# Kernel tuning notes

Measured on AMD Instinct MI355X. Metric: run time of the kernel, lower is better.

## Reference

```python
import jax, jax.numpy as jnp
import numpy as np

EPS = 1e-5
NUM_HEADS = 3


def _ln(x, g, b):
    m = jnp.mean(x, axis=-1, keepdims=True)
    v = jnp.mean((x - m) ** 2, axis=-1, keepdims=True)
    return (x - m) * jax.lax.rsqrt(v + EPS) * g + b


def setup_inputs() -> dict:
    key = jax.random.key(0)
    ks = jax.random.split(key, 8)
    Bn, N, C = 256, 197, 192           # graph nodes, tokens per node, embed_dim
    E = 1024                           # edges
    hid = int(C * 4.0)                 # mlp hidden
    def w(k, shape, fan_in):
        return (jax.random.normal(k, shape, jnp.float32) / np.sqrt(fan_in)).astype(jnp.float32)
    return {
        "x": jax.random.normal(ks[0], (Bn, N, C), jnp.float32),
        "egde": jax.random.randint(ks[1], (2, E), 0, Bn),
        "norm1_g": jnp.ones((C,), jnp.float32),
        "norm1_b": jnp.zeros((C,), jnp.float32),
        "qkv_w": w(ks[2], (3 * C, C), C),          # Linear(dim, 3*dim, bias=False)
        "proj_w": w(ks[3], (C, C), C),
        "proj_b": jnp.zeros((C,), jnp.float32),
        "norm2_g": jnp.ones((C,), jnp.float32),
        "norm2_b": jnp.zeros((C,), jnp.float32),
        "fc1_w": w(ks[4], (hid, C), C),
        "fc1_b": jnp.zeros((hid,), jnp.float32),
        "fc2_w": w(ks[5], (C, hid), hid),
        "fc2_b": jnp.zeros((C,), jnp.float32),
    }


def reference(x, egde, norm1_g, norm1_b, qkv_w, proj_w, proj_b,
              norm2_g, norm2_b, fc1_w, fc1_b, fc2_w, fc2_b):
    Bn, N, C = x.shape
    H = NUM_HEADS
    hd = C // H
    scale = hd ** -0.5

    # --- MEConv2 ---
    xn = _ln(x, norm1_g, norm1_b)
    qkv = (xn @ qkv_w.T).reshape(Bn, N, 3, H, hd)
    src, dst = egde[0], egde[1]        # x_j = source, aggregation index = target
    xi = qkv[dst]                      # [E, N, 3, H, hd]
    xj = qkv[src]
    q = xi[:, :, 0]                    # [E, N, H, hd] (from destination)
    v = xi[:, :, 2]                    # note: v comes from x_i, as in the source
    k = xj[:, :, 1]                    # key from source node
    attn = jnp.einsum('enhd,emhd->ehnm', q, k) * scale   # [E, H, N, N]
    attn = jax.nn.softmax(attn, axis=-1)
    msg = jnp.einsum('ehnm,emhd->enhd', attn, v).reshape(-1, N, C)
    msg = msg @ proj_w.T + proj_b      # [E, N, C]
    # scatter-mean over destination nodes (empty nodes -> 0, like torch scatter)
    agg = jax.ops.segment_sum(msg, dst, num_segments=Bn)
    cnt = jax.ops.segment_sum(jnp.ones(dst.shape, x.dtype), dst, num_segments=Bn)
    y = agg / jnp.maximum(cnt, 1.0)[:, None, None]

    # --- residual + MLP ---
    x = x + y
    h = _ln(x, norm2_g, norm2_b)
    h = jax.nn.gelu(h @ fc1_w.T + fc1_b, approximate=False)  # torch nn.GELU = exact
    h = h @ fc2_w.T + fc2_b
    return x + h
```

## Files before the change

### kernel.cpp

```cpp
#include <hip/hip_runtime.h>
#include <hip/hip_bf16.h>
#include <cstddef>


typedef __attribute__((ext_vector_type(8))) short bf8_t;
typedef __attribute__((ext_vector_type(4))) float f4_t;

__device__ __forceinline__ float bf2f(unsigned short u) {
  union { unsigned int i; float f; } x; x.i = ((unsigned int)u) << 16; return x.f;
}
__device__ __forceinline__ unsigned short f2bf(float f) {
  unsigned int u = __builtin_bit_cast(unsigned int, f);
  u = (u + 0x7FFFu + ((u >> 16) & 1u)) >> 16;
  return (unsigned short)u;
}
__device__ __forceinline__ unsigned int cvt_pk_bf16(float a, float b) {
  unsigned int r;
  asm("v_cvt_pk_bf16_f32 %0, %1, %2" : "=v"(r) : "v"(a), "v"(b));
  return r;
}

__global__ __launch_bounds__(256) void f2bf_kernel(const float* __restrict__ src,
                                                   unsigned short* __restrict__ dst, int n) {
  int i = blockIdx.x * 256 + threadIdx.x;
  if (i < n) dst[i] = f2bf(src[i]);
}

__global__ __launch_bounds__(256) void ln_bf16_kernel(const float* __restrict__ X,
    const float* __restrict__ g, const float* __restrict__ b,
    unsigned short* __restrict__ Y) {
  int row = blockIdx.x * 4 + (threadIdx.x >> 6);
  int lane = threadIdx.x & 63;
  const float* xr = X + (size_t)row * 192;
  float v0 = xr[lane], v1 = xr[lane + 64], v2 = xr[lane + 128];
  float s = v0 + v1 + v2, ss = v0 * v0 + v1 * v1 + v2 * v2;
#pragma unroll
  for (int o = 32; o > 0; o >>= 1) { s += __shfl_xor(s, o, 64); ss += __shfl_xor(ss, o, 64); }
  float mean = s * (1.f / 192.f);
  float var = ss * (1.f / 192.f) - mean * mean;
  float r = rsqrtf(var + 1e-5f);
  unsigned short* yr = Y + (size_t)row * 192;
  yr[lane]       = f2bf((v0 - mean) * r * g[lane]       + b[lane]);
  yr[lane + 64]  = f2bf((v1 - mean) * r * g[lane + 64]  + b[lane + 64]);
  yr[lane + 128] = f2bf((v2 - mean) * r * g[lane + 128] + b[lane + 128]);
}

template<int MODE, int NK>
__global__ __launch_bounds__(256) void gemm_bf16(
    const unsigned short* __restrict__ A, const unsigned short* __restrict__ W,
    const float* __restrict__ bias, const float* __restrict__ xres,
    const int* __restrict__ cntg, void* __restrict__ Cout,
    unsigned short* __restrict__ Cvt, int ldc) {
  constexpr int LDA = 200;
  __shared__ unsigned short As[128 * LDA];
  __shared__ unsigned short Ws[64 * LDA];
  const int tid = threadIdx.x;
  const int m0 = blockIdx.x * 128, n0 = blockIdx.y * 64;
  const int wave = tid >> 6, lane = tid & 63;
  const int mfrag = lane & 15, quad = lane >> 4;
  const int K = NK * 192;

  f4_t acc[2][4];
#pragma unroll
  for (int i = 0; i < 2; ++i)
#pragma unroll
    for (int j = 0; j < 4; ++j) acc[i][j] = (f4_t){0.f, 0.f, 0.f, 0.f};

  for (int kc = 0; kc < NK; ++kc) {
    __syncthreads();
#pragma unroll
    for (int it = 0; it < 12; ++it) {
      int idx = it * 256 + tid;
      int r = idx / 24, c = idx % 24;
      *(float4*)(As + r * LDA + c * 8) =
          *(const float4*)(A + (size_t)(m0 + r) * K + kc * 192 + c * 8);
    }
#pragma unroll
    for (int it = 0; it < 6; ++it) {
      int idx = it * 256 + tid;
      int r = idx / 24, c = idx % 24;
      *(float4*)(Ws + r * LDA + c * 8) =
          *(const float4*)(W + (size_t)(n0 + r) * K + kc * 192 + c * 8);
    }
    __syncthreads();
#pragma unroll
    for (int ks = 0; ks < 6; ++ks) {
      bf8_t a0 = *(const bf8_t*)(As + (wave * 32 + mfrag) * LDA + ks * 32 + quad * 8);
      bf8_t a1 = *(const bf8_t*)(As + (wave * 32 + 16 + mfrag) * LDA + ks * 32 + quad * 8);
#pragma unroll
      for (int nt = 0; nt < 4; ++nt) {
        bf8_t bf = *(const bf8_t*)(Ws + (nt * 16 + mfrag) * LDA + ks * 32 + quad * 8);
        acc[0][nt] = __builtin_amdgcn_mfma_f32_16x16x32_bf16(a0, bf, acc[0][nt], 0, 0, 0);
        acc[1][nt] = __builtin_amdgcn_mfma_f32_16x16x32_bf16(a1, bf, acc[1][nt], 0, 0, 0);
      }
    }
  }

#pragma unroll
  for (int mt = 0; mt < 2; ++mt)
#pragma unroll
    for (int nt = 0; nt < 4; ++nt)
#pragma unroll
      for (int reg = 0; reg < 4; ++reg) {
        int row = m0 + wave * 32 + mt * 16 + quad * 4 + reg;
        int col = n0 + nt * 16 + mfrag;
        float v = acc[mt][nt][reg];
        if constexpr (MODE == 0) {
          if (col < 384) {
            ((unsigned short*)Cout)[(size_t)row * 384 + col] = f2bf(v);
          } else {
            int cc = col - 384, hh = cc >> 6, dd = cc & 63;
            int bb = row / 197, tt = row - bb * 197;
            Cvt[((size_t)(bb * 3 + hh) * 64 + dd) * 200 + tt] = f2bf(v);
          }
        } else if constexpr (MODE == 1) {
          int c = cntg[row / 197];
          v = (c > 0) ? v / (float)c + bias[col] : 0.f;
          v += xres[(size_t)row * 192 + col];
          ((float*)Cout)[(size_t)row * ldc + col] = v;
        } else if constexpr (MODE == 2) {
          v += bias[col];
          v = 0.5f * v * (1.f + erff(v * 0.70710678118654752f));
          ((unsigned short*)Cout)[(size_t)row * ldc + col] = f2bf(v);
        } else {
          v += bias[col] + xres[(size_t)row * 192 + col];
          ((float*)Cout)[(size_t)row * ldc + col] = v;
        }
      }
}

__global__ __launch_bounds__(512) void attnA_kernel(
    const unsigned short* __restrict__ qk, const unsigned short* __restrict__ vtg,
    const int* __restrict__ edge, unsigned short* __restrict__ msgbuf) {
  const int e = blockIdx.x, h = blockIdx.y;
  const int s = edge[e], b = edge[1024 + e];
  __shared__ unsigned short Ks[208 * 72];
  __shared__ unsigned short Vt[64 * 232];
  __shared__ unsigned short Ps[8][640];
  const int tid = threadIdx.x;
  const int wave = tid >> 6, lane = tid & 63;
  const int mfrag = lane & 15, quad = lane >> 4;

  for (int i = tid; i < 197 * 8; i += 512) {
    int m = i >> 3, c8 = i & 7;
    *(float4*)(Ks + m * 72 + c8 * 8) =
        *(const float4*)(qk + (size_t)(s * 197 + m) * 384 + 192 + h * 64 + c8 * 8);
  }
  for (int i = tid; i < 64 * 25; i += 512) {
    int d = i / 25, c8 = i - d * 25;
    *(float4*)(Vt + d * 232 + c8 * 8) =
        *(const float4*)(vtg + ((size_t)(b * 3 + h) * 64 + d) * 200 + c8 * 8);
  }
  __syncthreads();
  for (int i = tid; i < 64 * 35; i += 512) {
    int d = i / 35, kk = 197 + (i - d * 35);
    Vt[d * 232 + kk] = 0;
  }
  __syncthreads();

  for (int st = wave; st < 13; st += 8) {
    const int m0 = st * 16;
    const size_t qrow = (size_t)(b * 197 + min(m0 + mfrag, 196)) * 384 + h * 64;
    bf8_t a0 = *(const bf8_t*)(qk + qrow + quad * 8);
    bf8_t a1 = *(const bf8_t*)(qk + qrow + 32 + quad * 8);

    f4_t S[13];
#pragma unroll
    for (int nt = 0; nt < 13; ++nt) {
      bf8_t k0 = *(const bf8_t*)(Ks + (nt * 16 + mfrag) * 72 + quad * 8);
      bf8_t k1 = *(const bf8_t*)(Ks + (nt * 16 + mfrag) * 72 + 32 + quad * 8);
      f4_t z = (f4_t){0.f, 0.f, 0.f, 0.f};
      z = __builtin_amdgcn_mfma_f32_16x16x32_bf16(a0, k0, z, 0, 0, 0);
      S[nt] = __builtin_amdgcn_mfma_f32_16x16x32_bf16(a1, k1, z, 0, 0, 0);
    }

#pragma unroll
    for (int reg = 0; reg < 4; ++reg)
      S[12][reg] = (mfrag < 5) ? S[12][reg] : -1e30f;

    float mx[4] = {-1e30f, -1e30f, -1e30f, -1e30f};
#pragma unroll
    for (int nt = 0; nt < 13; ++nt)
#pragma unroll
      for (int reg = 0; reg < 4; ++reg) mx[reg] = fmaxf(mx[reg], S[nt][reg]);
#pragma unroll
    for (int off = 1; off < 16; off <<= 1)
#pragma unroll
      for (int reg = 0; reg < 4; ++reg) mx[reg] = fmaxf(mx[reg], __shfl_xor(mx[reg], off, 64));

    constexpr float CEXP = 0.18033688011112042f;
    float sum[4] = {0.f, 0.f, 0.f, 0.f};
#pragma unroll
    for (int nt = 0; nt < 13; ++nt)
#pragma unroll
      for (int reg = 0; reg < 4; ++reg) {
        float p = exp2f((S[nt][reg] - mx[reg]) * CEXP);
        S[nt][reg] = p;
        sum[reg] += p;
      }
#pragma unroll
    for (int off = 1; off < 16; off <<= 1)
#pragma unroll
      for (int reg = 0; reg < 4; ++reg) sum[reg] += __shfl_xor(sum[reg], off, 64);
    float inv[4];
#pragma unroll
    for (int reg = 0; reg < 4; ++reg) inv[reg] = __builtin_amdgcn_rcpf(sum[reg]);

    f4_t o[4];
#pragma unroll
    for (int dt = 0; dt < 4; ++dt) o[dt] = (f4_t){0.f, 0.f, 0.f, 0.f};
    unsigned short* buf = Ps[wave];
#pragma unroll
    for (int kt = 0; kt < 7; ++kt) {
#pragma unroll
      for (int reg = 0; reg < 4; ++reg) {
        float p0 = S[kt * 2][reg];
        float p1 = (kt * 2 + 1 < 13) ? S[kt * 2 + 1][reg] : 0.f;
        unsigned int u = cvt_pk_bf16(p0, p1);
        buf[(quad * 4 + reg) * 40 + mfrag]      = (unsigned short)u;
        buf[(quad * 4 + reg) * 40 + 16 + mfrag] = (unsigned short)(u >> 16);
      }
      bf8_t pf = *(const bf8_t*)(buf + mfrag * 40 + quad * 8);
#pragma unroll
      for (int dt = 0; dt < 4; ++dt) {
        bf8_t vf = *(const bf8_t*)(Vt + (dt * 16 + mfrag) * 232 + kt * 32 + quad * 8);
        o[dt] = __builtin_amdgcn_mfma_f32_16x16x32_bf16(pf, vf, o[dt], 0, 0, 0);
      }
    }

#pragma unroll
    for (int dt = 0; dt < 4; dt += 2)
#pragma unroll
      for (int reg = 0; reg < 4; ++reg) {
        int q = m0 + quad * 4 + reg;
        unsigned int u = cvt_pk_bf16(o[dt][reg] * inv[reg], o[dt + 1][reg] * inv[reg]);
        if (q < 197) {
          size_t base = (size_t)e * 37824 + q * 192 + h * 64 + dt * 16 + mfrag;
          msgbuf[base]      = (unsigned short)u;
          msgbuf[base + 16] = (unsigned short)(u >> 16);
        }
      }
  }
}

__global__ __launch_bounds__(256) void aggregate_kernel(
    const unsigned short* __restrict__ msgbuf, const int* __restrict__ edge,
    unsigned short* __restrict__ agg, int* __restrict__ cntg) {
  const int b = blockIdx.x, chunk = blockIdx.y;
  __shared__ int list[1024];
  __shared__ int lc;
  const int tid = threadIdx.x;
  if (tid == 0) lc = 0;
  __syncthreads();
  for (int e = tid; e < 1024; e += 256)
    if (edge[1024 + e] == b) { int p = atomicAdd(&lc, 1); list[p] = e; }
  __syncthreads();
  const int cnt = lc;
  if (chunk == 0 && tid == 0) cntg[b] = cnt;
  const int base = chunk * 9456;
  for (int i8 = tid; i8 < 1182; i8 += 256) {
    int i = base + i8 * 8;
    float sum[8];
#pragma unroll
    for (int kk = 0; kk < 8; ++kk) sum[kk] = 0.f;
    for (int j = 0; j < cnt; ++j) {
      float4 t = *(const float4*)(msgbuf + (size_t)list[j] * 37824 + i);
      const unsigned short* u = (const unsigned short*)&t;
#pragma unroll
      for (int kk = 0; kk < 8; ++kk) sum[kk] += bf2f(u[kk]);
    }
    unsigned short o[8];
#pragma unroll
    for (int kk = 0; kk < 8; ++kk) o[kk] = f2bf(sum[kk]);
    *(float4*)(agg + (size_t)b * 37824 + i) = *(const float4*)o;
  }
}

extern "C" void kernel_launch(void* const* d_in, const int* in_sizes, int n_in,
                              void* d_out, int out_size, void* d_ws, size_t ws_size,
                              hipStream_t stream) {
  const float* x      = (const float*)d_in[0];
  const int*   edge   = (const int*)d_in[1];
  const float* n1g    = (const float*)d_in[2];
  const float* n1b    = (const float*)d_in[3];
  const float* qkv_w  = (const float*)d_in[4];
  const float* proj_w = (const float*)d_in[5];
  const float* proj_b = (const float*)d_in[6];
  const float* n2g    = (const float*)d_in[7];
  const float* n2b    = (const float*)d_in[8];
  const float* fc1_w  = (const float*)d_in[9];
  const float* fc1_b  = (const float*)d_in[10];
  const float* fc2_w  = (const float*)d_in[11];
  const float* fc2_b  = (const float*)d_in[12];
  float* out = (float*)d_out;

  char* ws = (char*)d_ws;
  unsigned short* msgbuf = (unsigned short*)ws;
  unsigned short* h1     = (unsigned short*)ws;
  unsigned short* qk     = (unsigned short*)(ws + 77463552);
  unsigned short* xn     = (unsigned short*)(ws + 116195328);
  unsigned short* agg    = (unsigned short*)(ws + 135561216);
  unsigned short* vtg    = (unsigned short*)(ws + 154927104);
  unsigned short* wqkv   = (unsigned short*)(ws + 174587904);
  unsigned short* wproj  = (unsigned short*)(ws + 174809088);
  unsigned short* wfc1   = (unsigned short*)(ws + 174882816);
  unsigned short* wfc2   = (unsigned short*)(ws + 175177728);
  int*            cntg   = (int*)           (ws + 175472640);

  dim3 blk(256);
  f2bf_kernel<<<dim3(432), blk, 0, stream>>>(qkv_w, wqkv, 110592);
  f2bf_kernel<<<dim3(144), blk, 0, stream>>>(proj_w, wproj, 36864);
  f2bf_kernel<<<dim3(576), blk, 0, stream>>>(fc1_w, wfc1, 147456);
  f2bf_kernel<<<dim3(576), blk, 0, stream>>>(fc2_w, wfc2, 147456);

  ln_bf16_kernel<<<dim3(12608), blk, 0, stream>>>(x, n1g, n1b, xn);
  gemm_bf16<0, 1><<<dim3(394, 9), blk, 0, stream>>>(xn, wqkv, nullptr, nullptr, nullptr, qk, vtg, 384);
  attnA_kernel<<<dim3(1024, 3), dim3(512), 0, stream>>>(qk, vtg, edge, msgbuf);
  aggregate_kernel<<<dim3(256, 4), blk, 0, stream>>>(msgbuf, edge, agg, cntg);
  gemm_bf16<1, 1><<<dim3(394, 3), blk, 0, stream>>>(agg, wproj, proj_b, x, cntg, out, nullptr, 192);
  ln_bf16_kernel<<<dim3(12608), blk, 0, stream>>>(out, n2g, n2b, xn);
  gemm_bf16<2, 1><<<dim3(394, 12), blk, 0, stream>>>(xn, wfc1, fc1_b, nullptr, nullptr, h1, nullptr, 768);
  gemm_bf16<3, 4><<<dim3(394, 3), blk, 0, stream>>>(h1, wfc2, fc2_b, out, nullptr, out, nullptr, 192);
}
```

Measured before the change: 477.3 us.

## Fuse scatter-mean into attention via float atomics, drop message buffer

The attention kernel now atomically adds normalized outputs straight into a float32 per-node aggregation buffer. This replaces the per-edge bf16 message buffer and the separate aggregate kernel, and a small kernel computes the in-degree counts. The proj GEMM reads the fp32 aggregate and converts it to bf16 while loading. Softmax row reductions switch from shuffles to DPP row rotations, and GEMM grids are swapped so N tiles vary fastest for better A reuse. The cost is a memset of the aggregate buffer, atomic contention on high-degree nodes, and nondeterministic summation order.

Result: slower. 544.5 us (+14.1%).

```diff
diff --git a/kernel.cpp b/kernel.cpp
--- a/kernel.cpp
+++ b/kernel.cpp
@@ -19,11 +19,27 @@
   asm("v_cvt_pk_bf16_f32 %0, %1, %2" : "=v"(r) : "v"(a), "v"(b));
   return r;
 }
+template<int CTRL>
+__device__ __forceinline__ float dpp_ror(float x) {
+  return __builtin_bit_cast(float,
+      __builtin_amdgcn_mov_dpp(__builtin_bit_cast(int, x), CTRL, 0xF, 0xF, false));
+}
 
 __global__ __launch_bounds__(256) void f2bf_kernel(const float* __restrict__ src,
                                                    unsigned short* __restrict__ dst, int n) {
   int i = blockIdx.x * 256 + threadIdx.x;
   if (i < n) dst[i] = f2bf(src[i]);
+}
+
+__global__ __launch_bounds__(256) void cnt_kernel(const int* __restrict__ edge,
+                                                  int* __restrict__ cntg) {
+  __shared__ int c[256];
+  int t = threadIdx.x;
+  c[t] = 0;
+  __syncthreads();
+  for (int e = t; e < 1024; e += 256) atomicAdd(&c[edge[1024 + e]], 1);
+  __syncthreads();
+  cntg[t] = c[t];
 }
 
 __global__ __launch_bounds__(256) void ln_bf16_kernel(const float* __restrict__ X,
@@ -45,9 +61,10 @@
   yr[lane + 128] = f2bf((v2 - mean) * r * g[lane + 128] + b[lane + 128]);
 }
 
-template<int MODE, int NK>
+template<int MODE, int NK, bool AF32 = false>
 __global__ __launch_bounds__(256) void gemm_bf16(
-    const unsigned short* __restrict__ A, const unsigned short* __restrict__ W,
+    const unsigned short* __restrict__ A, const float* __restrict__ Af,
+    const unsigned short* __restrict__ W,
     const float* __restrict__ bias, const float* __restrict__ xres,
     const int* __restrict__ cntg, void* __restrict__ Cout,
     unsigned short* __restrict__ Cvt, int ldc) {
@@ -55,7 +72,7 @@
   __shared__ unsigned short As[128 * LDA];
   __shared__ unsigned short Ws[64 * LDA];
   const int tid = threadIdx.x;
-  const int m0 = blockIdx.x * 128, n0 = blockIdx.y * 64;
+  const int m0 = blockIdx.y * 128, n0 = blockIdx.x * 64;
   const int wave = tid >> 6, lane = tid & 63;
   const int mfrag = lane & 15, quad = lane >> 4;
   const int K = NK * 192;
@@ -68,12 +85,25 @@
 
   for (int kc = 0; kc < NK; ++kc) {
     __syncthreads();
-#pragma unroll
-    for (int it = 0; it < 12; ++it) {
-      int idx = it * 256 + tid;
-      int r = idx / 24, c = idx % 24;
-      *(float4*)(As + r * LDA + c * 8) =
-          *(const float4*)(A + (size_t)(m0 + r) * K + kc * 192 + c * 8);
+    if constexpr (AF32) {
+#pragma unroll
+      for (int it = 0; it < 24; ++it) {
+        int idx = it * 256 + tid;
+        int r = idx / 48, c = idx % 48;
+        float4 t = *(const float4*)(Af + (size_t)(m0 + r) * K + kc * 192 + c * 4);
+        unsigned int u0 = cvt_pk_bf16(t.x, t.y);
+        unsigned int u1 = cvt_pk_bf16(t.z, t.w);
+        uint2 p; p.x = u0; p.y = u1;
+        *(uint2*)(As + r * LDA + c * 4) = p;
+      }
+    } else {
+#pragma unroll
+      for (int it = 0; it < 12; ++it) {
+        int idx = it * 256 + tid;
+        int r = idx / 24, c = idx % 24;
+        *(float4*)(As + r * LDA + c * 8) =
+            *(const float4*)(A + (size_t)(m0 + r) * K + kc * 192 + c * 8);
+      }
     }
 #pragma unroll
     for (int it = 0; it < 6; ++it) {
@@ -131,7 +161,7 @@
 
 __global__ __launch_bounds__(512) void attnA_kernel(
     const unsigned short* __restrict__ qk, const unsigned short* __restrict__ vtg,
-    const int* __restrict__ edge, unsigned short* __restrict__ msgbuf) {
+    const int* __restrict__ edge, float* __restrict__ aggF) {
   const int e = blockIdx.x, h = blockIdx.y;
   const int s = edge[e], b = edge[1024 + e];
   __shared__ unsigned short Ks[208 * 72];
@@ -184,9 +214,12 @@
 #pragma unroll
       for (int reg = 0; reg < 4; ++reg) mx[reg] = fmaxf(mx[reg], S[nt][reg]);
 #pragma unroll
-    for (int off = 1; off < 16; off <<= 1)
-#pragma unroll
-      for (int reg = 0; reg < 4; ++reg) mx[reg] = fmaxf(mx[reg], __shfl_xor(mx[reg], off, 64));
+    for (int reg = 0; reg < 4; ++reg) {
+      mx[reg] = fmaxf(mx[reg], dpp_ror<0x121>(mx[reg]));
+      mx[reg] = fmaxf(mx[reg], dpp_ror<0x122>(mx[reg]));
+      mx[reg] = fmaxf(mx[reg], dpp_ror<0x124>(mx[reg]));
+      mx[reg] = fmaxf(mx[reg], dpp_ror<0x128>(mx[reg]));
+    }
 
     constexpr float CEXP = 0.18033688011112042f;
     float sum[4] = {0.f, 0.f, 0.f, 0.f};
@@ -199,9 +232,12 @@
         sum[reg] += p;
       }
 #pragma unroll
-    for (int off = 1; off < 16; off <<= 1)
-#pragma unroll
-      for (int reg = 0; reg < 4; ++reg) sum[reg] += __shfl_xor(sum[reg], off, 64);
+    for (int reg = 0; reg < 4; ++reg) {
+      sum[reg] += dpp_ror<0x121>(sum[reg]);
+      sum[reg] += dpp_ror<0x122>(sum[reg]);
+      sum[reg] += dpp_ror<0x124>(sum[reg]);
+      sum[reg] += dpp_ror<0x128>(sum[reg]);
+    }
     float inv[4];
 #pragma unroll
     for (int reg = 0; reg < 4; ++reg) inv[reg] = __builtin_amdgcn_rcpf(sum[reg]);
@@ -229,50 +265,14 @@
     }
 
 #pragma unroll
-    for (int dt = 0; dt < 4; dt += 2)
+    for (int dt = 0; dt < 4; ++dt)
 #pragma unroll
       for (int reg = 0; reg < 4; ++reg) {
         int q = m0 + quad * 4 + reg;
-        unsigned int u = cvt_pk_bf16(o[dt][reg] * inv[reg], o[dt + 1][reg] * inv[reg]);
-        if (q < 197) {
-          size_t base = (size_t)e * 37824 + q * 192 + h * 64 + dt * 16 + mfrag;
-          msgbuf[base]      = (unsigned short)u;
-          msgbuf[base + 16] = (unsigned short)(u >> 16);
-        }
-      }
-  }
-}
-
-__global__ __launch_bounds__(256) void aggregate_kernel(
-    const unsigned short* __restrict__ msgbuf, const int* __restrict__ edge,
-    unsigned short* __restrict__ agg, int* __restrict__ cntg) {
-  const int b = blockIdx.x, chunk = blockIdx.y;
-  __shared__ int list[1024];
-  __shared__ int lc;
-  const int tid = threadIdx.x;
-  if (tid == 0) lc = 0;
-  __syncthreads();
-  for (int e = tid; e < 1024; e += 256)
-    if (edge[1024 + e] == b) { int p = atomicAdd(&lc, 1); list[p] = e; }
-  __syncthreads();
-  const int cnt = lc;
-  if (chunk == 0 && tid == 0) cntg[b] = cnt;
-  const int base = chunk * 9456;
-  for (int i8 = tid; i8 < 1182; i8 += 256) {
-    int i = base + i8 * 8;
-    float sum[8];
-#pragma unroll
-    for (int kk = 0; kk < 8; ++kk) sum[kk] = 0.f;
-    for (int j = 0; j < cnt; ++j) {
-      float4 t = *(const float4*)(msgbuf + (size_t)list[j] * 37824 + i);
-      const unsigned short* u = (const unsigned short*)&t;
-#pragma unroll
-      for (int kk = 0; kk < 8; ++kk) sum[kk] += bf2f(u[kk]);
-    }
-    unsigned short o[8];
-#pragma unroll
-    for (int kk = 0; kk < 8; ++kk) o[kk] = f2bf(sum[kk]);
-    *(float4*)(agg + (size_t)b * 37824 + i) = *(const float4*)o;
+        if (q < 197)
+          unsafeAtomicAdd(&aggF[((size_t)b * 197 + q) * 192 + h * 64 + dt * 16 + mfrag],
+                          o[dt][reg] * inv[reg]);
+      }
   }
 }
 
@@ -295,11 +295,10 @@
   float* out = (float*)d_out;
 
   char* ws = (char*)d_ws;
-  unsigned short* msgbuf = (unsigned short*)ws;
+  float*          aggF   = (float*)ws;
   unsigned short* h1     = (unsigned short*)ws;
   unsigned short* qk     = (unsigned short*)(ws + 77463552);
   unsigned short* xn     = (unsigned short*)(ws + 116195328);
-  unsigned short* agg    = (unsigned short*)(ws + 135561216);
   unsigned short* vtg    = (unsigned short*)(ws + 154927104);
   unsigned short* wqkv   = (unsigned short*)(ws + 174587904);
   unsigned short* wproj  = (unsigned short*)(ws + 174809088);
@@ -308,17 +307,18 @@
   int*            cntg   = (int*)           (ws + 175472640);
 
   dim3 blk(256);
+  hipMemsetAsync(aggF, 0, 38731776, stream);
   f2bf_kernel<<<dim3(432), blk, 0, stream>>>(qkv_w, wqkv, 110592);
   f2bf_kernel<<<dim3(144), blk, 0, stream>>>(proj_w, wproj, 36864);
   f2bf_kernel<<<dim3(576), blk, 0, stream>>>(fc1_w, wfc1, 147456);
   f2bf_kernel<<<dim3(576), blk, 0, stream>>>(fc2_w, wfc2, 147456);
+  cnt_kernel<<<dim3(1), blk, 0, stream>>>(edge, cntg);
 
   ln_bf16_kernel<<<dim3(12608), blk, 0, stream>>>(x, n1g, n1b, xn);
-  gemm_bf16<0, 1><<<dim3(394, 9), blk, 0, stream>>>(xn, wqkv, nullptr, nullptr, nullptr, qk, vtg, 384);
-  attnA_kernel<<<dim3(1024, 3), dim3(512), 0, stream>>>(qk, vtg, edge, msgbuf);
-  aggregate_kernel<<<dim3(256, 4), blk, 0, stream>>>(msgbuf, edge, agg, cntg);
-  gemm_bf16<1, 1><<<dim3(394, 3), blk, 0, stream>>>(agg, wproj, proj_b, x, cntg, out, nullptr, 192);
+  gemm_bf16<0, 1><<<dim3(9, 394), blk, 0, stream>>>(xn, nullptr, wqkv, nullptr, nullptr, nullptr, qk, vtg, 384);
+  attnA_kernel<<<dim3(1024, 3), dim3(512), 0, stream>>>(qk, vtg, edge, aggF);
+  gemm_bf16<1, 1, true><<<dim3(3, 394), blk, 0, stream>>>(nullptr, aggF, wproj, proj_b, x, cntg, out, nullptr, 192);
   ln_bf16_kernel<<<dim3(12608), blk, 0, stream>>>(out, n2g, n2b, xn);
-  gemm_bf16<2, 1><<<dim3(394, 12), blk, 0, stream>>>(xn, wfc1, fc1_b, nullptr, nullptr, h1, nullptr, 768);
-  gemm_bf16<3, 4><<<dim3(394, 3), blk, 0, stream>>>(h1, wfc2, fc2_b, out, nullptr, out, nullptr, 192);
-}
+  gemm_bf16<2, 1><<<dim3(12, 394), blk, 0, stream>>>(xn, nullptr, wfc1, fc1_b, nullptr, nullptr, h1, nullptr, 768);
+  gemm_bf16<3, 4><<<dim3(3, 394), blk, 0, stream>>>(h1, nullptr, wfc2, fc2_b, out, nullptr, out, nullptr, 192);
+}
```

## Permute V layout for packed P stores, use DPP row reductions, swap GEMM grid order

Applied to the files above, without the earlier changes.

The V-transpose written by the QKV GEMM is reordered within 32-token chunks so the attention kernel can store softmax probabilities as packed 32-bit pairs instead of two 16-bit stores. The max and sum reductions across 16 lanes switch from shuffle-xor to DPP row-rotate operations, avoiding LDS-backed shuffles. The GEMM grids are transposed so blocks sharing the same M tile run next to each other, aiming for better reuse of the A tile in L2. The V permutation and P packing must stay consistent, which adds risk.

Measured after the change: 510.9 us. +7.0%, slower.

```diff
diff --git a/kernel.cpp b/kernel.cpp
--- a/kernel.cpp
+++ b/kernel.cpp
@@ -18,6 +18,11 @@
   unsigned int r;
   asm("v_cvt_pk_bf16_f32 %0, %1, %2" : "=v"(r) : "v"(a), "v"(b));
   return r;
+}
+template<int CTRL>
+__device__ __forceinline__ float dpp_ror(float x) {
+  return __builtin_bit_cast(float,
+      __builtin_amdgcn_mov_dpp(__builtin_bit_cast(int, x), CTRL, 0xF, 0xF, false));
 }
 
 __global__ __launch_bounds__(256) void f2bf_kernel(const float* __restrict__ src,
@@ -55,7 +60,7 @@
   __shared__ unsigned short As[128 * LDA];
   __shared__ unsigned short Ws[64 * LDA];
   const int tid = threadIdx.x;
-  const int m0 = blockIdx.x * 128, n0 = blockIdx.y * 64;
+  const int m0 = blockIdx.y * 128, n0 = blockIdx.x * 64;
   const int wave = tid >> 6, lane = tid & 63;
   const int mfrag = lane & 15, quad = lane >> 4;
   const int K = NK * 192;
@@ -111,7 +116,9 @@
           } else {
             int cc = col - 384, hh = cc >> 6, dd = cc & 63;
             int bb = row / 197, tt = row - bb * 197;
-            Cvt[((size_t)(bb * 3 + hh) * 64 + dd) * 200 + tt] = f2bf(v);
+            int c5 = tt >> 5, w = tt & 31;
+            int pos = (c5 < 6) ? c5 * 32 + 2 * (w & 15) + (w >> 4) : tt;
+            Cvt[((size_t)(bb * 3 + hh) * 64 + dd) * 200 + pos] = f2bf(v);
           }
         } else if constexpr (MODE == 1) {
           int c = cntg[row / 197];
@@ -184,9 +191,12 @@
 #pragma unroll
       for (int reg = 0; reg < 4; ++reg) mx[reg] = fmaxf(mx[reg], S[nt][reg]);
 #pragma unroll
-    for (int off = 1; off < 16; off <<= 1)
-#pragma unroll
-      for (int reg = 0; reg < 4; ++reg) mx[reg] = fmaxf(mx[reg], __shfl_xor(mx[reg], off, 64));
+    for (int reg = 0; reg < 4; ++reg) {
+      mx[reg] = fmaxf(mx[reg], dpp_ror<0x121>(mx[reg]));
+      mx[reg] = fmaxf(mx[reg], dpp_ror<0x122>(mx[reg]));
+      mx[reg] = fmaxf(mx[reg], dpp_ror<0x124>(mx[reg]));
+      mx[reg] = fmaxf(mx[reg], dpp_ror<0x128>(mx[reg]));
+    }
 
     constexpr float CEXP = 0.18033688011112042f;
     float sum[4] = {0.f, 0.f, 0.f, 0.f};
@@ -199,9 +209,12 @@
         sum[reg] += p;
       }
 #pragma unroll
-    for (int off = 1; off < 16; off <<= 1)
-#pragma unroll
-      for (int reg = 0; reg < 4; ++reg) sum[reg] += __shfl_xor(sum[reg], off, 64);
+    for (int reg = 0; reg < 4; ++reg) {
+      sum[reg] += dpp_ror<0x121>(sum[reg]);
+      sum[reg] += dpp_ror<0x122>(sum[reg]);
+      sum[reg] += dpp_ror<0x124>(sum[reg]);
+      sum[reg] += dpp_ror<0x128>(sum[reg]);
+    }
     float inv[4];
 #pragma unroll
     for (int reg = 0; reg < 4; ++reg) inv[reg] = __builtin_amdgcn_rcpf(sum[reg]);
@@ -212,13 +225,19 @@
     unsigned short* buf = Ps[wave];
 #pragma unroll
     for (int kt = 0; kt < 7; ++kt) {
-#pragma unroll
-      for (int reg = 0; reg < 4; ++reg) {
-        float p0 = S[kt * 2][reg];
-        float p1 = (kt * 2 + 1 < 13) ? S[kt * 2 + 1][reg] : 0.f;
-        unsigned int u = cvt_pk_bf16(p0, p1);
-        buf[(quad * 4 + reg) * 40 + mfrag]      = (unsigned short)u;
-        buf[(quad * 4 + reg) * 40 + 16 + mfrag] = (unsigned short)(u >> 16);
+      if (kt < 6) {
+#pragma unroll
+        for (int reg = 0; reg < 4; ++reg) {
+          unsigned int u = cvt_pk_bf16(S[kt * 2][reg], S[kt * 2 + 1][reg]);
+          *(unsigned int*)(buf + (quad * 4 + reg) * 40 + 2 * mfrag) = u;
+        }
+      } else {
+#pragma unroll
+        for (int reg = 0; reg < 4; ++reg) {
+          unsigned int u = cvt_pk_bf16(S[12][reg], 0.f);
+          buf[(quad * 4 + reg) * 40 + mfrag]      = (unsigned short)u;
+          buf[(quad * 4 + reg) * 40 + 16 + mfrag] = 0;
+        }
       }
       bf8_t pf = *(const bf8_t*)(buf + mfrag * 40 + quad * 8);
 #pragma unroll
@@ -314,11 +333,11 @@
   f2bf_kernel<<<dim3(576), blk, 0, stream>>>(fc2_w, wfc2, 147456);
 
   ln_bf16_kernel<<<dim3(12608), blk, 0, stream>>>(x, n1g, n1b, xn);
-  gemm_bf16<0, 1><<<dim3(394, 9), blk, 0, stream>>>(xn, wqkv, nullptr, nullptr, nullptr, qk, vtg, 384);
+  gemm_bf16<0, 1><<<dim3(9, 394), blk, 0, stream>>>(xn, wqkv, nullptr, nullptr, nullptr, qk, vtg, 384);
   attnA_kernel<<<dim3(1024, 3), dim3(512), 0, stream>>>(qk, vtg, edge, msgbuf);
   aggregate_kernel<<<dim3(256, 4), blk, 0, stream>>>(msgbuf, edge, agg, cntg);
-  gemm_bf16<1, 1><<<dim3(394, 3), blk, 0, stream>>>(agg, wproj, proj_b, x, cntg, out, nullptr, 192);
+  gemm_bf16<1, 1><<<dim3(3, 394), blk, 0, stream>>>(agg, wproj, proj_b, x, cntg, out, nullptr, 192);
   ln_bf16_kernel<<<dim3(12608), blk, 0, stream>>>(out, n2g, n2b, xn);
-  gemm_bf16<2, 1><<<dim3(394, 12), blk, 0, stream>>>(xn, wfc1, fc1_b, nullptr, nullptr, h1, nullptr, 768);
-  gemm_bf16<3, 4><<<dim3(394, 3), blk, 0, stream>>>(h1, wfc2, fc2_b, out, nullptr, out, nullptr, 192);
-}
+  gemm_bf16<2, 1><<<dim3(12, 394), blk, 0, stream>>>(xn, wfc1, fc1_b, nullptr, nullptr, h1, nullptr, 768);
+  gemm_bf16<3, 4><<<dim3(3, 394), blk, 0, stream>>>(h1, wfc2, fc2_b, out, nullptr, out, nullptr, 192);
+}
```
